# Kernel tuning notes

Hardware: AMD Instinct MI355X
Metric: run time of the kernel (lower is better)

The kernel has to match this reference:

```python
import jax, jax.numpy as jnp
import numpy as np
import math

DIM = 1024
NUM_HEADS = 16
HEAD_DIM = 64
NUM_FEATURES = 128
B, N = 2, 1024


def _sample_orf(rng, num_features, head_dim):
    # Orthogonal Random Features: stack QR-orthogonalized blocks scaled by chi(D) row norms
    blocks = []
    while len(blocks) * head_dim < num_features:
        G = rng.standard_normal((head_dim, head_dim)).astype(np.float32)
        Q, _ = np.linalg.qr(G)
        norms = np.linalg.norm(rng.standard_normal((head_dim, head_dim)).astype(np.float32), axis=1)
        blocks.append(np.diag(norms) @ Q.T)
    return np.concatenate(blocks, axis=0)[:num_features]


def setup_inputs() -> dict:
    key = jax.random.key(0)
    ks = jax.random.split(key, 6)
    s = 1.0 / math.sqrt(DIM)
    x = jax.random.normal(ks[0], (B, N, DIM), dtype=jnp.float32)
    omega = jnp.asarray(_sample_orf(np.random.default_rng(0), NUM_FEATURES, HEAD_DIM))
    Wq = jax.random.normal(ks[1], (DIM, DIM), dtype=jnp.float32) * s
    Wk = jax.random.normal(ks[2], (DIM, DIM), dtype=jnp.float32) * s
    Wv = jax.random.normal(ks[3], (DIM, DIM), dtype=jnp.float32) * s
    Wo = jax.random.normal(ks[4], (DIM, DIM), dtype=jnp.float32) * s
    bo = jax.random.normal(ks[5], (DIM,), dtype=jnp.float32) * 0.01
    return {"x": x, "omega": omega, "Wq": Wq, "Wk": Wk, "Wv": Wv, "Wo": Wo, "bo": bo}


def _phi(x, omega, is_query):
    # x: [B,H,N,D], omega: [M,D] -> [B,H,N,M]
    proj = jnp.einsum('bhnd,md->bhnm', x, omega)
    norm = 0.5 * jnp.sum(x * x, axis=-1, keepdims=True)
    log_phi = proj - norm
    if is_query:
        log_phi = log_phi - jnp.max(log_phi, axis=-1, keepdims=True)
    else:
        log_phi = log_phi - jnp.max(log_phi)
    return jnp.exp(log_phi) / math.sqrt(NUM_FEATURES) + 1e-4


def reference(x, omega, Wq, Wk, Wv, Wo, bo):
    Bx, Nx, _ = x.shape
    H, D = NUM_HEADS, HEAD_DIM

    def split_heads(y):  # [B,N,H*D] -> [B,H,N,D]
        return y.reshape(Bx, Nx, H, D).transpose(0, 2, 1, 3)

    q = split_heads(x @ Wq.T)
    k = split_heads(x @ Wk.T)
    v = split_heads(x @ Wv.T)

    scale = D ** (-0.25)
    phi_q = _phi(q * scale, omega, is_query=True)   # [B,H,N,M]
    phi_k = _phi(k * scale, omega, is_query=False)  # [B,H,N,M]

    # causal linear attention via explicit kv outer-product cumsum (as in source)
    kv = jnp.einsum('bhnm,bhnd->bhnmd', phi_k, v)
    kv_cumsum = jnp.cumsum(kv, axis=2)              # [B,H,N,M,D]
    k_cumsum = jnp.cumsum(phi_k, axis=2)            # [B,H,N,M]
    out = jnp.einsum('bhnm,bhnmd->bhnd', phi_q, kv_cumsum)
    z = 1.0 / (jnp.einsum('bhnm,bhnm->bhn', phi_q, k_cumsum) + 1e-6)
    out = out * z[..., None]

    out = out.transpose(0, 2, 1, 3).reshape(Bx, Nx, H * D)
    return out @ Wo.T + bo
```

## Files before the change

kernel.cpp:

```cpp
#include <hip/hip_runtime.h>
#include <hip/hip_bf16.h>
#include <math.h>

#define DIMS 1024
#define NHEADS 16
#define HDIM 64
#define NFEAT 128
#define BB 2
#define NN 1024
#define BN (BB*NN)
#define NCH 16
#define CSZ 64
#define WW (DIMS*DIMS)
#define QKVN (3*DIMS)

#define SCALE 0.3535533905932738f
#define INV_SQRT_M 0.08838834764831845f

typedef __attribute__((ext_vector_type(8))) _Float16 h8v;
typedef __attribute__((ext_vector_type(8))) short s8v;
typedef __attribute__((ext_vector_type(4))) float f4v;

__device__ __forceinline__ ushort f2h(float x) {
    _Float16 h = (_Float16)x;
    return *(ushort*)&h;
}
__device__ __forceinline__ float h2f(ushort u) {
    _Float16 h = *(_Float16*)&u;
    return (float)h;
}
__device__ __forceinline__ void gload16(const void* g, void* l) {
    __builtin_amdgcn_global_load_lds(
        (const __attribute__((address_space(1))) unsigned int*)g,
        (__attribute__((address_space(3))) unsigned int*)l,
        16, 0, 0);
}

#define NX (BN*DIMS/8)
#define NW (WW/8)
#define NOM (NFEAT*HDIM/8)
__global__ __launch_bounds__(256) void cast_all(const float* __restrict__ x,
                                                const float* __restrict__ Wq,
                                                const float* __restrict__ Wk,
                                                const float* __restrict__ Wv,
                                                const float* __restrict__ Wo,
                                                const float* __restrict__ omega,
                                                ushort* __restrict__ xh,
                                                ushort* __restrict__ wqkvh,
                                                ushort* __restrict__ woh,
                                                ushort* __restrict__ omh) {
    const int i = blockIdx.x * 256 + threadIdx.x;
    const float* src; ushort* dst; int off;
    if (i < NX)               { src = x;     dst = xh;                     off = i; }
    else if (i < NX + NW)     { src = Wq;    dst = wqkvh;                  off = i - NX; }
    else if (i < NX + 2 * NW) { src = Wk;    dst = wqkvh + WW;             off = i - NX - NW; }
    else if (i < NX + 3 * NW) { src = Wv;    dst = wqkvh + 2 * (size_t)WW; off = i - NX - 2 * NW; }
    else if (i < NX + 4 * NW) { src = Wo;    dst = woh;                    off = i - NX - 3 * NW; }
    else                      { src = omega; dst = omh;                    off = i - NX - 4 * NW; }
    float4 a = ((const float4*)src)[2 * (size_t)off];
    float4 b = ((const float4*)src)[2 * (size_t)off + 1];
    float v[8] = {a.x, a.y, a.z, a.w, b.x, b.y, b.z, b.w};
    ushort h8[8];
    #pragma unroll
    for (int j = 0; j < 8; ++j) h8[j] = f2h(v[j]);
    *(s8v*)&dst[(size_t)off * 8] = *(s8v*)&h8[0];
}

template<int BM, bool HOUT>
__global__ __launch_bounds__(256) void gemm_nt_lds(const ushort* __restrict__ A,
                                                   const ushort* __restrict__ B,
                                                   float* __restrict__ C,
                                                   ushort* __restrict__ C16,
                                                   const float* __restrict__ bias,
                                                   int M, int N, int K, int nbx) {
    constexpr int MF = BM / 32;
    constexpr int AI = BM / 64;
    __shared__ __attribute__((aligned(16))) ushort lA[BM][32];
    __shared__ __attribute__((aligned(16))) ushort lB[128][32];
    const int tid = threadIdx.x;
    const int w = tid >> 6, l = tid & 63, lr = l & 15, lg = l >> 4;
    const int wm = (w >> 1) * (BM / 2), wn = (w & 1) * 64;
    const int nwg = gridDim.x;
    const int q8 = nwg >> 3;
    const int neu = (blockIdx.x & 7) * q8 + (blockIdx.x >> 3);
    const int bx = neu % nbx, by = neu / nbx;
    const int bi = bx * BM, bj = by * 128;
    const int srow = l >> 2, scol = (l & 3) * 8;

    f4v acc[MF][4] = {};
    for (int k0 = 0; k0 < K; k0 += 32) {
        #pragma unroll
        for (int i = 0; i < AI; ++i) {
            const int r0 = w * (16 * AI) + i * 16;
            gload16(&A[(size_t)(bi + r0 + srow) * K + k0 + scol], &lA[r0][0]);
        }
        #pragma unroll
        for (int i = 0; i < 2; ++i) {
            const int r0 = w * 32 + i * 16;
            gload16(&B[(size_t)(bj + r0 + srow) * K + k0 + scol], &lB[r0][0]);
        }
        __syncthreads();
        h8v b_[4];
        #pragma unroll
        for (int j = 0; j < 4; ++j) b_[j] = *(h8v*)&lB[wn + j * 16 + lr][lg * 8];
        #pragma unroll
        for (int i = 0; i < MF; ++i) {
            h8v a_ = *(h8v*)&lA[wm + i * 16 + lr][lg * 8];
            #pragma unroll
            for (int j = 0; j < 4; ++j)
                acc[i][j] = __builtin_amdgcn_mfma_f32_16x16x32_f16(a_, b_[j], acc[i][j], 0, 0, 0);
        }
        __syncthreads();
    }
    #pragma unroll
    for (int i = 0; i < MF; ++i)
        #pragma unroll
        for (int j = 0; j < 4; ++j)
            #pragma unroll
            for (int rg = 0; rg < 4; ++rg) {
                const int row = bi + wm + i * 16 + lg * 4 + rg;
                const int col = bj + wn + j * 16 + lr;
                if (HOUT) {
                    C16[(size_t)row * N + col] = f2h(acc[i][j][rg]);
                } else {
                    float r = acc[i][j][rg] + bias[col];
                    C[(size_t)row * N + col] = r;
                }
            }
}

__global__ __launch_bounds__(256) void phi_mfma(const ushort* __restrict__ qkvh,
                                                const ushort* __restrict__ omh,
                                                ushort* __restrict__ phiq,
                                                ushort* __restrict__ plocal,
                                                float* __restrict__ blockmax,
                                                ushort* __restrict__ vt,
                                                ushort* __restrict__ ssum16,
                                                float* __restrict__ kcsum,
                                                float* __restrict__ vsum) {
    __shared__ __attribute__((aligned(16))) ushort lq[64][72];
    __shared__ __attribute__((aligned(16))) ushort lom[128 * 72];
    __shared__ __attribute__((aligned(16))) ushort lktT[128][72];
    __shared__ __attribute__((aligned(16))) ushort lv[64][72];
    __shared__ __attribute__((aligned(16))) ushort lvt[64][72];
    __shared__ float lnorm[64];
    __shared__ float wred[4];
    const int tid = threadIdx.x;
    const int z = blockIdx.z, h = blockIdx.y;
    const int bn0 = blockIdx.x * 64;
    const int w = tid >> 6, l = tid & 63, lr = l & 15, lg = l >> 4;
    const int b = blockIdx.x >> 4, c = blockIdx.x & 15;
    const int bh = b * NHEADS + h;

    {
        const int r = tid >> 2, c0 = (tid & 3) * 16;
        const size_t g = (size_t)(bn0 + r) * QKVN + (size_t)z * DIMS + h * HDIM + c0;
        s8v v0 = *(const s8v*)&qkvh[g];
        s8v v1 = *(const s8v*)&qkvh[g + 8];
        *(s8v*)&lq[r][c0] = v0;
        *(s8v*)&lq[r][c0 + 8] = v1;
        float p = 0.f;
        #pragma unroll
        for (int j = 0; j < 8; ++j) {
            float a = h2f(((ushort*)&v0)[j]); p += a * a;
            float bb2 = h2f(((ushort*)&v1)[j]); p += bb2 * bb2;
        }
        p += __shfl_xor(p, 1); p += __shfl_xor(p, 2);
        if ((tid & 3) == 0) lnorm[r] = p;
    }
    {
        const int m = tid >> 1, c0 = (tid & 1) * 32;
        #pragma unroll
        for (int i = 0; i < 4; ++i)
            *(s8v*)&lom[m * 72 + c0 + i * 8] = *(const s8v*)&omh[m * HDIM + c0 + i * 8];
    }
    if (z == 1) {
        const int r = tid >> 2, c0 = (tid & 3) * 16;
        const size_t g = (size_t)(bn0 + r) * QKVN + 2 * DIMS + h * HDIM + c0;
        *(s8v*)&lv[r][c0]     = *(const s8v*)&qkvh[g];
        *(s8v*)&lv[r][c0 + 8] = *(const s8v*)&qkvh[g + 8];
    }
    __syncthreads();

    f4v acc[8] = {};
    #pragma unroll
    for (int k0 = 0; k0 < 64; k0 += 32) {
        h8v a = *(h8v*)&lq[w * 16 + lr][k0 + lg * 8];
        #pragma unroll
        for (int ct = 0; ct < 8; ++ct) {
            h8v bo = *(h8v*)&lom[(ct * 16 + lr) * 72 + k0 + lg * 8];
            acc[ct] = __builtin_amdgcn_mfma_f32_16x16x32_f16(a, bo, acc[ct], 0, 0, 0);
        }
    }

    const float hs2 = 0.5f * SCALE * SCALE;
    float lvv[4][8];
    #pragma unroll
    for (int rg = 0; rg < 4; ++rg) {
        const int row = w * 16 + lg * 4 + rg;
        const float nh = hs2 * lnorm[row];
        #pragma unroll
        for (int ct = 0; ct < 8; ++ct) lvv[rg][ct] = SCALE * acc[ct][rg] - nh;
    }
    if (z == 1) {
        float bmax = -3.4e38f;
        #pragma unroll
        for (int rg = 0; rg < 4; ++rg)
            #pragma unroll
            for (int ct = 0; ct < 8; ++ct) bmax = fmaxf(bmax, lvv[rg][ct]);
        #pragma unroll
        for (int o = 32; o >= 1; o >>= 1) bmax = fmaxf(bmax, __shfl_xor(bmax, o));
        if (l == 0) wred[w] = bmax;
    }
    __syncthreads();

    if (z == 0) {
        #pragma unroll
        for (int rg = 0; rg < 4; ++rg) {
            const int row = w * 16 + lg * 4 + rg;
            float mx = -3.4e38f;
            #pragma unroll
            for (int ct = 0; ct < 8; ++ct) mx = fmaxf(mx, lvv[rg][ct]);
            #pragma unroll
            for (int o = 8; o >= 1; o >>= 1) mx = fmaxf(mx, __shfl_xor(mx, o));
            #pragma unroll
            for (int ct = 0; ct < 8; ++ct)
                lom[row * 136 + ct * 16 + lr] = f2h(expf(lvv[rg][ct] - mx) * INV_SQRT_M + 1e-4f);
        }
    } else {
        const float bm = fmaxf(fmaxf(wred[0], wred[1]), fmaxf(wred[2], wred[3]));
        if (tid == 0) blockmax[h * 32 + blockIdx.x] = bm;
        #pragma unroll
        for (int rg = 0; rg < 4; ++rg) {
            const int row = w * 16 + lg * 4 + rg;
            #pragma unroll
            for (int ct = 0; ct < 8; ++ct)
                lom[row * 136 + ct * 16 + lr] = f2h(expf(lvv[rg][ct] - bm));
        }
    }
    __syncthreads();

    {
        ushort* dst = (z == 0) ? phiq : plocal;
        const int r = tid >> 2, c0 = (tid & 3) * 32;
        const size_t orow = ((size_t)bh * NN + (blockIdx.x & 15) * 64 + ((bn0 >> 10) ? 0 : 0)
                             + ((size_t)0)) * 0;
        const int br = bn0 + r;
        const int bb2 = br >> 10, n = br & (NN - 1);
        const size_t og = ((size_t)(bb2 * NHEADS + h) * NN + n) * NFEAT;
        #pragma unroll
        for (int i = 0; i < 4; ++i)
            *(s8v*)&dst[og + c0 + i * 8] = *(s8v*)&lom[r * 136 + c0 + i * 8];
        (void)orow;
    }
    if (z == 0) return;

    {
        const int m = tid >> 1, nh2 = (tid & 1) * 32;
        ushort tp[32];
        #pragma unroll
        for (int i = 0; i < 32; ++i) tp[i] = lom[(nh2 + i) * 136 + m];
        #pragma unroll
        for (int i = 0; i < 4; ++i) *(s8v*)&lktT[m][nh2 + i * 8] = *(s8v*)&tp[i * 8];
    }
    {
        const int d = tid >> 2, s0 = (tid & 3) * 16;
        ushort tp[16];
        #pragma unroll
        for (int i = 0; i < 16; ++i) tp[i] = lv[s0 + i][d];
        const size_t tb = ((size_t)bh * HDIM + d) * NN + c * CSZ + (b ? 0 : 0) + s0;
        *(s8v*)&vt[((size_t)bh * HDIM + d) * NN + c * CSZ + s0] = *(s8v*)&tp[0];
        *(s8v*)&vt[((size_t)bh * HDIM + d) * NN + c * CSZ + s0 + 8] = *(s8v*)&tp[8];
        *(s8v*)&lvt[d][s0] = *(s8v*)&tp[0];
        *(s8v*)&lvt[d][s0 + 8] = *(s8v*)&tp[8];
        (void)tb;
    }
    __syncthreads();

    f4v ac2[8] = {};
    #pragma unroll
    for (int k0 = 0; k0 < 64; k0 += 32) {
        h8v a = *(h8v*)&lvt[w * 16 + lr][k0 + lg * 8];
        #pragma unroll
        for (int ct = 0; ct < 8; ++ct) {
            h8v bf = *(h8v*)&lktT[ct * 16 + lr][k0 + lg * 8];
            ac2[ct] = __builtin_amdgcn_mfma_f32_16x16x32_f16(a, bf, ac2[ct], 0, 0, 0);
        }
    }
    const size_t obase = ((size_t)bh * NCH + c) * (HDIM * NFEAT);
    #pragma unroll
    for (int ct = 0; ct < 8; ++ct)
        #pragma unroll
        for (int rg = 0; rg < 4; ++rg) {
            const int d = w * 16 + lg * 4 + rg, m = ct * 16 + lr;
            ssum16[obase + (size_t)d * NFEAT + m] = f2h(ac2[ct][rg]);
        }
    if (tid < 128) {
        float s = 0.f;
        #pragma unroll 8
        for (int i = 0; i < 64; ++i) s += h2f(lktT[tid][i]);
        kcsum[((size_t)bh * NCH + c) * NFEAT + tid] = s;
    }
    if (tid < 64) {
        float s = 0.f;
        #pragma unroll 8
        for (int i = 0; i < 64; ++i) s += h2f(lvt[tid][i]);
        vsum[((size_t)bh * NCH + c) * HDIM + tid] = s;
    }
}

__global__ __launch_bounds__(256) void chunk_prefix(const ushort* __restrict__ ssum16,
                                                    ushort* __restrict__ spre,
                                                    const float* __restrict__ kcsum,
                                                    float* __restrict__ kcpre,
                                                    const float* __restrict__ blockmax,
                                                    const float* __restrict__ vsum) {
    const int bh = blockIdx.y, sl = blockIdx.x;
    const int tid = threadIdx.x;
    const int b = bh >> 4, h = bh & 15;
    __shared__ float gred[4];
    float mx = fmaxf(blockmax[tid], blockmax[tid + 256]);
    #pragma unroll
    for (int o = 32; o >= 1; o >>= 1) mx = fmaxf(mx, __shfl_xor(mx, o));
    if ((tid & 63) == 0) gred[tid >> 6] = mx;
    __syncthreads();
    const float gm = fmaxf(fmaxf(gred[0], gred[1]), fmaxf(gred[2], gred[3]));

    if (sl == 0 && tid < NFEAT) {
        float a = 0.f;
        for (int c = 0; c < NCH; ++c) {
            kcpre[((size_t)bh * NCH + c) * NFEAT + tid] = a;
            const float fac = expf(blockmax[h * 32 + b * 16 + c] - gm) * INV_SQRT_M;
            a += fac * kcsum[((size_t)bh * NCH + c) * NFEAT + tid] + 64.0f * 1e-4f;
        }
    }
    const int base_e = (sl * 256 + tid) * 8;
    const int d = base_e >> 7;
    float acc[8] = {};
    const size_t bb = (size_t)bh * NCH * (HDIM * NFEAT);
    for (int c = 0; c < NCH; ++c) {
        const size_t cb = bb + (size_t)c * (HDIM * NFEAT);
        const float fac = expf(blockmax[h * 32 + b * 16 + c] - gm) * INV_SQRT_M;
        const float vs = vsum[((size_t)bh * NCH + c) * HDIM + d];
        s8v v = *(const s8v*)&ssum16[cb + base_e];
        ushort o[8];
        #pragma unroll
        for (int j = 0; j < 8; ++j) o[j] = f2h(acc[j]);
        *(s8v*)&spre[cb + base_e] = *(s8v*)&o[0];
        #pragma unroll
        for (int j = 0; j < 8; ++j) acc[j] += fac * h2f(((ushort*)&v)[j]) + 1e-4f * vs;
    }
}

__global__ __launch_bounds__(256) void scan_final(const ushort* __restrict__ phiq,
                                                  const ushort* __restrict__ plocal,
                                                  const ushort* __restrict__ vt,
                                                  const ushort* __restrict__ spre,
                                                  const float* __restrict__ kcpre,
                                                  const float* __restrict__ blockmax,
                                                  ushort* __restrict__ att_h) {
    const int c = blockIdx.x, bh = blockIdx.y;
    const int b = bh >> 4, h = bh & 15;
    const int n0 = c * CSZ;
    __shared__ __attribute__((aligned(16))) ushort lq[64][136];
    __shared__ __attribute__((aligned(16))) ushort lk[64][136];
    __shared__ __attribute__((aligned(16))) ushort lvt[64][72];
    __shared__ __attribute__((aligned(16))) ushort lsp[64][136];
    __shared__ __attribute__((aligned(16))) ushort lA[64][72];
    __shared__ float kc[NFEAT];
    __shared__ float zin[64];
    __shared__ float zp[4][64];
    __shared__ float gred[4];
    const int tid = threadIdx.x;

    float mxv = fmaxf(blockmax[tid], blockmax[tid + 256]);
    #pragma unroll
    for (int o = 32; o >= 1; o >>= 1) mxv = fmaxf(mxv, __shfl_xor(mxv, o));
    if ((tid & 63) == 0) gred[tid >> 6] = mxv;
    __syncthreads();
    const float gm = fmaxf(fmaxf(gred[0], gred[1]), fmaxf(gred[2], gred[3]));
    const float fac = expf(blockmax[h * 32 + b * 16 + c] - gm) * INV_SQRT_M;

    const size_t qb = ((size_t)bh * NN + n0) * NFEAT;
    #pragma unroll
    for (int i = 0; i < 4; ++i) {
        const int idx = tid + 256 * i;
        const int r = idx >> 4, cs = (idx & 15) * 8;
        *(s8v*)&lq[r][cs] = *(const s8v*)&phiq[qb + (size_t)r * NFEAT + cs];
        s8v pv = *(const s8v*)&plocal[qb + (size_t)r * NFEAT + cs];
        ushort t[8];
        #pragma unroll
        for (int j = 0; j < 8; ++j) t[j] = f2h(h2f(((ushort*)&pv)[j]) * fac + 1e-4f);
        *(s8v*)&lk[r][cs] = *(s8v*)&t[0];
    }
    const size_t sb = ((size_t)bh * NCH + c) * (HDIM * NFEAT);
    #pragma unroll
    for (int i = 0; i < 4; ++i) {
        const int idx = tid + 256 * i;
        const int r = idx >> 4, cs = (idx & 15) * 8;
        *(s8v*)&lsp[r][cs] = *(const s8v*)&spre[sb + (size_t)r * NFEAT + cs];
    }
    {
        const int d = tid >> 2, s = (tid & 3) * 16;
        const size_t g = ((size_t)bh * HDIM + d) * NN + n0 + s;
        *(s8v*)&lvt[d][s]     = *(const s8v*)&vt[g];
        *(s8v*)&lvt[d][s + 8] = *(const s8v*)&vt[g + 8];
    }
    if (tid < NFEAT) kc[tid] = kcpre[((size_t)bh * NCH + c) * NFEAT + tid];
    __syncthreads();

    const int w = tid >> 6, l = tid & 63, lr = l & 15, lg = l >> 4;

    f4v a4[4] = {};
    #pragma unroll
    for (int k0 = 0; k0 < 128; k0 += 32) {
        h8v av = *(h8v*)&lq[w * 16 + lr][k0 + lg * 8];
        #pragma unroll
        for (int ct = 0; ct < 4; ++ct) {
            h8v bv = *(h8v*)&lk[ct * 16 + lr][k0 + lg * 8];
            a4[ct] = __builtin_amdgcn_mfma_f32_16x16x32_f16(av, bv, a4[ct], 0, 0, 0);
        }
    }
    float zi[4] = {0.f, 0.f, 0.f, 0.f};
    #pragma unroll
    for (int ct = 0; ct < 4; ++ct) {
        #pragma unroll
        for (int rg = 0; rg < 4; ++rg) {
            const int row = w * 16 + lg * 4 + rg;
            const int col = ct * 16 + lr;
            const float val = (col <= row) ? a4[ct][rg] : 0.f;
            const ushort hq = f2h(val);
            zi[rg] += h2f(hq);
            lA[row][col] = hq;
        }
    }
    #pragma unroll
    for (int rg = 0; rg < 4; ++rg) {
        float z = zi[rg];
        z += __shfl_xor(z, 1); z += __shfl_xor(z, 2);
        z += __shfl_xor(z, 4); z += __shfl_xor(z, 8);
        if (lr == 0) zin[w * 16 + lg * 4 + rg] = z;
    }
    {
        const int row = tid & 63, qq = tid >> 6;
        float s = 0.f;
        #pragma unroll 8
        for (int m = 0; m < 32; ++m) s += h2f(lq[row][qq * 32 + m]) * kc[qq * 32 + m];
        zp[qq][row] = s;
    }
    __syncthreads();

    f4v o4[4] = {};
    #pragma unroll
    for (int k0 = 0; k0 < 64; k0 += 32) {
        h8v av = *(h8v*)&lA[w * 16 + lr][k0 + lg * 8];
        #pragma unroll
        for (int ct = 0; ct < 4; ++ct) {
            h8v bv = *(h8v*)&lvt[ct * 16 + lr][k0 + lg * 8];
            o4[ct] = __builtin_amdgcn_mfma_f32_16x16x32_f16(av, bv, o4[ct], 0, 0, 0);
        }
    }
    #pragma unroll
    for (int k0 = 0; k0 < 128; k0 += 32) {
        h8v av = *(h8v*)&lq[w * 16 + lr][k0 + lg * 8];
        #pragma unroll
        for (int ct = 0; ct < 4; ++ct) {
            h8v bv = *(h8v*)&lsp[ct * 16 + lr][k0 + lg * 8];
            o4[ct] = __builtin_amdgcn_mfma_f32_16x16x32_f16(av, bv, o4[ct], 0, 0, 0);
        }
    }
    #pragma unroll
    for (int rg = 0; rg < 4; ++rg) {
        const int row = w * 16 + lg * 4 + rg;
        const float z = zin[row] + zp[0][row] + zp[1][row] + zp[2][row] + zp[3][row] + 1e-6f;
        const float rz = 1.f / z;
        #pragma unroll
        for (int ct = 0; ct < 4; ++ct) {
            const int d = ct * 16 + lr;
            att_h[((size_t)(b * NN + n0 + row)) * DIMS + h * HDIM + d] = f2h(o4[ct][rg] * rz);
        }
    }
}

extern "C" void kernel_launch(void* const* d_in, const int* in_sizes, int n_in,
                              void* d_out, int out_size, void* d_ws, size_t ws_size,
                              hipStream_t stream) {
    const float* x     = (const float*)d_in[0];
    const float* omega = (const float*)d_in[1];
    const float* Wq    = (const float*)d_in[2];
    const float* Wk    = (const float*)d_in[3];
    const float* Wv    = (const float*)d_in[4];
    const float* Wo    = (const float*)d_in[5];
    const float* bo    = (const float*)d_in[6];
    float* out = (float*)d_out;

    const size_t PROJ = (size_t)BN * DIMS;
    const size_t PHI  = (size_t)BB * NHEADS * NN * NFEAT;
    ushort* qkvh    = (ushort*)d_ws;
    ushort* xh      = qkvh + (size_t)BN * QKVN;
    ushort* wqkvh   = xh + PROJ;
    ushort* woh     = wqkvh + (size_t)QKVN * DIMS;
    ushort* omh     = woh + WW;
    ushort* phiq_h  = omh + NFEAT * HDIM;
    ushort* plocal  = phiq_h + PHI;
    ushort* vt_h    = plocal + PHI;
    ushort* ssum16  = vt_h + PROJ;
    ushort* spre_h  = ssum16 + PHI;
    ushort* att_hb  = spre_h + PHI;
    float*  kcsum   = (float*)(att_hb + PROJ);
    float*  kcpre   = kcsum + 32 * NCH * NFEAT;
    float*  blockmax= kcpre + 32 * NCH * NFEAT;
    float*  vsum    = blockmax + 512;

    cast_all<<<(NX + 4 * NW + NOM) / 256, 256, 0, stream>>>(x, Wq, Wk, Wv, Wo, omega,
                                                            xh, wqkvh, woh, omh);

    gemm_nt_lds<64, true><<<(BN / 64) * (QKVN / 128), 256, 0, stream>>>(
        xh, wqkvh, nullptr, qkvh, nullptr, BN, QKVN, DIMS, BN / 64);

    dim3 pg(BN / 64, NHEADS, 2);
    phi_mfma<<<pg, 256, 0, stream>>>(qkvh, omh, phiq_h, plocal, blockmax,
                                     vt_h, ssum16, kcsum, vsum);

    chunk_prefix<<<dim3(4, BB * NHEADS), 256, 0, stream>>>(ssum16, spre_h, kcsum, kcpre,
                                                           blockmax, vsum);
    dim3 cg(NCH, BB * NHEADS);
    scan_final<<<cg, 256, 0, stream>>>(phiq_h, plocal, vt_h, spre_h, kcpre,
                                       blockmax, att_hb);

    gemm_nt_lds<64, false><<<(BN / 64) * (DIMS / 128), 256, 0, stream>>>(
        att_hb, woh, out, nullptr, bo, BN, DIMS, DIMS, BN / 64);
}
```

Baseline: 89.02 us.

## Fuse chunk prefix into scan_final and widen GEMM K-tile with swizzled LDS

Removes the separate chunk_prefix kernel: each scan_final block now recomputes its own exclusive prefix of the chunk state sums and key sums directly from ssum16/kcsum, saving a launch and the spre/kcpre round trip through memory. The price is redundant work, since later chunks re-read and accumulate up to 15 prior chunk states, which adds quadratic reads and per-thread register pressure (32 float accumulators). Separately, the GEMM K-tile is doubled from 32 to 64 with an XOR-swizzled LDS layout to halve barriers per K and cut bank conflicts. Some dead address code is also cleaned up.

```diff
diff --git a/kernel.cpp b/kernel.cpp
--- a/kernel.cpp
+++ b/kernel.cpp
@@ -74,9 +74,9 @@
                                                    const float* __restrict__ bias,
                                                    int M, int N, int K, int nbx) {
     constexpr int MF = BM / 32;
-    constexpr int AI = BM / 64;
-    __shared__ __attribute__((aligned(16))) ushort lA[BM][32];
-    __shared__ __attribute__((aligned(16))) ushort lB[128][32];
+    constexpr int AI = BM / 32;
+    __shared__ __attribute__((aligned(16))) ushort lA[BM][64];
+    __shared__ __attribute__((aligned(16))) ushort lB[128][64];
     const int tid = threadIdx.x;
     const int w = tid >> 6, l = tid & 63, lr = l & 15, lg = l >> 4;
     const int wm = (w >> 1) * (BM / 2), wn = (w & 1) * 64;
@@ -85,30 +85,35 @@
     const int neu = (blockIdx.x & 7) * q8 + (blockIdx.x >> 3);
     const int bx = neu % nbx, by = neu / nbx;
     const int bi = bx * BM, bj = by * 128;
-    const int srow = l >> 2, scol = (l & 3) * 8;
+    const int srow = l >> 3;
+    const int scol = ((l & 7) ^ (l >> 3)) * 8;
 
     f4v acc[MF][4] = {};
-    for (int k0 = 0; k0 < K; k0 += 32) {
+    for (int k0 = 0; k0 < K; k0 += 64) {
         #pragma unroll
         for (int i = 0; i < AI; ++i) {
-            const int r0 = w * (16 * AI) + i * 16;
+            const int r0 = w * (8 * AI) + i * 8;
             gload16(&A[(size_t)(bi + r0 + srow) * K + k0 + scol], &lA[r0][0]);
         }
         #pragma unroll
-        for (int i = 0; i < 2; ++i) {
-            const int r0 = w * 32 + i * 16;
+        for (int i = 0; i < 4; ++i) {
+            const int r0 = w * 32 + i * 8;
             gload16(&B[(size_t)(bj + r0 + srow) * K + k0 + scol], &lB[r0][0]);
         }
         __syncthreads();
-        h8v b_[4];
-        #pragma unroll
-        for (int j = 0; j < 4; ++j) b_[j] = *(h8v*)&lB[wn + j * 16 + lr][lg * 8];
-        #pragma unroll
-        for (int i = 0; i < MF; ++i) {
-            h8v a_ = *(h8v*)&lA[wm + i * 16 + lr][lg * 8];
-            #pragma unroll
-            for (int j = 0; j < 4; ++j)
-                acc[i][j] = __builtin_amdgcn_mfma_f32_16x16x32_f16(a_, b_[j], acc[i][j], 0, 0, 0);
+        #pragma unroll
+        for (int kk = 0; kk < 2; ++kk) {
+            const int soff = ((kk * 4 + lg) ^ (lr & 7)) * 8;
+            h8v b_[4];
+            #pragma unroll
+            for (int j = 0; j < 4; ++j) b_[j] = *(h8v*)&lB[wn + j * 16 + lr][soff];
+            #pragma unroll
+            for (int i = 0; i < MF; ++i) {
+                h8v a_ = *(h8v*)&lA[wm + i * 16 + lr][soff];
+                #pragma unroll
+                for (int j = 0; j < 4; ++j)
+                    acc[i][j] = __builtin_amdgcn_mfma_f32_16x16x32_f16(a_, b_[j], acc[i][j], 0, 0, 0);
+            }
         }
         __syncthreads();
     }
@@ -243,15 +248,12 @@
     {
         ushort* dst = (z == 0) ? phiq : plocal;
         const int r = tid >> 2, c0 = (tid & 3) * 32;
-        const size_t orow = ((size_t)bh * NN + (blockIdx.x & 15) * 64 + ((bn0 >> 10) ? 0 : 0)
-                             + ((size_t)0)) * 0;
         const int br = bn0 + r;
         const int bb2 = br >> 10, n = br & (NN - 1);
         const size_t og = ((size_t)(bb2 * NHEADS + h) * NN + n) * NFEAT;
         #pragma unroll
         for (int i = 0; i < 4; ++i)
             *(s8v*)&dst[og + c0 + i * 8] = *(s8v*)&lom[r * 136 + c0 + i * 8];
-        (void)orow;
     }
     if (z == 0) return;
 
@@ -268,12 +270,11 @@
         ushort tp[16];
         #pragma unroll
         for (int i = 0; i < 16; ++i) tp[i] = lv[s0 + i][d];
-        const size_t tb = ((size_t)bh * HDIM + d) * NN + c * CSZ + (b ? 0 : 0) + s0;
-        *(s8v*)&vt[((size_t)bh * HDIM + d) * NN + c * CSZ + s0] = *(s8v*)&tp[0];
-        *(s8v*)&vt[((size_t)bh * HDIM + d) * NN + c * CSZ + s0 + 8] = *(s8v*)&tp[8];
+        const size_t tb = ((size_t)bh * HDIM + d) * NN + c * CSZ + s0;
+        *(s8v*)&vt[tb] = *(s8v*)&tp[0];
+        *(s8v*)&vt[tb + 8] = *(s8v*)&tp[8];
         *(s8v*)&lvt[d][s0] = *(s8v*)&tp[0];
         *(s8v*)&lvt[d][s0 + 8] = *(s8v*)&tp[8];
-        (void)tb;
     }
     __syncthreads();
 
@@ -309,54 +310,12 @@
     }
 }
 
-__global__ __launch_bounds__(256) void chunk_prefix(const ushort* __restrict__ ssum16,
-                                                    ushort* __restrict__ spre,
-                                                    const float* __restrict__ kcsum,
-                                                    float* __restrict__ kcpre,
-                                                    const float* __restrict__ blockmax,
-                                                    const float* __restrict__ vsum) {
-    const int bh = blockIdx.y, sl = blockIdx.x;
-    const int tid = threadIdx.x;
-    const int b = bh >> 4, h = bh & 15;
-    __shared__ float gred[4];
-    float mx = fmaxf(blockmax[tid], blockmax[tid + 256]);
-    #pragma unroll
-    for (int o = 32; o >= 1; o >>= 1) mx = fmaxf(mx, __shfl_xor(mx, o));
-    if ((tid & 63) == 0) gred[tid >> 6] = mx;
-    __syncthreads();
-    const float gm = fmaxf(fmaxf(gred[0], gred[1]), fmaxf(gred[2], gred[3]));
-
-    if (sl == 0 && tid < NFEAT) {
-        float a = 0.f;
-        for (int c = 0; c < NCH; ++c) {
-            kcpre[((size_t)bh * NCH + c) * NFEAT + tid] = a;
-            const float fac = expf(blockmax[h * 32 + b * 16 + c] - gm) * INV_SQRT_M;
-            a += fac * kcsum[((size_t)bh * NCH + c) * NFEAT + tid] + 64.0f * 1e-4f;
-        }
-    }
-    const int base_e = (sl * 256 + tid) * 8;
-    const int d = base_e >> 7;
-    float acc[8] = {};
-    const size_t bb = (size_t)bh * NCH * (HDIM * NFEAT);
-    for (int c = 0; c < NCH; ++c) {
-        const size_t cb = bb + (size_t)c * (HDIM * NFEAT);
-        const float fac = expf(blockmax[h * 32 + b * 16 + c] - gm) * INV_SQRT_M;
-        const float vs = vsum[((size_t)bh * NCH + c) * HDIM + d];
-        s8v v = *(const s8v*)&ssum16[cb + base_e];
-        ushort o[8];
-        #pragma unroll
-        for (int j = 0; j < 8; ++j) o[j] = f2h(acc[j]);
-        *(s8v*)&spre[cb + base_e] = *(s8v*)&o[0];
-        #pragma unroll
-        for (int j = 0; j < 8; ++j) acc[j] += fac * h2f(((ushort*)&v)[j]) + 1e-4f * vs;
-    }
-}
-
 __global__ __launch_bounds__(256) void scan_final(const ushort* __restrict__ phiq,
                                                   const ushort* __restrict__ plocal,
                                                   const ushort* __restrict__ vt,
-                                                  const ushort* __restrict__ spre,
-                                                  const float* __restrict__ kcpre,
+                                                  const ushort* __restrict__ ssum16,
+                                                  const float* __restrict__ kcsum,
+                                                  const float* __restrict__ vsum,
                                                   const float* __restrict__ blockmax,
                                                   ushort* __restrict__ att_h) {
     const int c = blockIdx.x, bh = blockIdx.y;
@@ -393,12 +352,36 @@
         for (int j = 0; j < 8; ++j) t[j] = f2h(h2f(((ushort*)&pv)[j]) * fac + 1e-4f);
         *(s8v*)&lk[r][cs] = *(s8v*)&t[0];
     }
-    const size_t sb = ((size_t)bh * NCH + c) * (HDIM * NFEAT);
-    #pragma unroll
-    for (int i = 0; i < 4; ++i) {
-        const int idx = tid + 256 * i;
-        const int r = idx >> 4, cs = (idx & 15) * 8;
-        *(s8v*)&lsp[r][cs] = *(const s8v*)&spre[sb + (size_t)r * NFEAT + cs];
+    {
+        const int d = tid >> 2;
+        const int m0 = (tid & 3) * 32;
+        float acc[32] = {};
+        float vs_tot = 0.f;
+        for (int cp = 0; cp < c; ++cp) {
+            const float facp = expf(blockmax[h * 32 + b * 16 + cp] - gm) * INV_SQRT_M;
+            vs_tot += vsum[((size_t)bh * NCH + cp) * HDIM + d];
+            const size_t cb = ((size_t)bh * NCH + cp) * (HDIM * NFEAT) + (size_t)d * NFEAT + m0;
+            #pragma unroll
+            for (int i = 0; i < 4; ++i) {
+                s8v v = *(const s8v*)&ssum16[cb + i * 8];
+                #pragma unroll
+                for (int j = 0; j < 8; ++j) acc[i * 8 + j] += facp * h2f(((ushort*)&v)[j]);
+            }
+        }
+        const float vadd = 1e-4f * vs_tot;
+        ushort o[32];
+        #pragma unroll
+        for (int i = 0; i < 32; ++i) o[i] = f2h(acc[i] + vadd);
+        #pragma unroll
+        for (int i = 0; i < 4; ++i) *(s8v*)&lsp[d][m0 + i * 8] = *(s8v*)&o[i * 8];
+    }
+    if (tid < NFEAT) {
+        float a = 0.f;
+        for (int cp = 0; cp < c; ++cp) {
+            const float facp = expf(blockmax[h * 32 + b * 16 + cp] - gm) * INV_SQRT_M;
+            a += facp * kcsum[((size_t)bh * NCH + cp) * NFEAT + tid] + 64.0f * 1e-4f;
+        }
+        kc[tid] = a;
     }
     {
         const int d = tid >> 2, s = (tid & 3) * 16;
@@ -406,7 +389,6 @@
         *(s8v*)&lvt[d][s]     = *(const s8v*)&vt[g];
         *(s8v*)&lvt[d][s + 8] = *(const s8v*)&vt[g + 8];
     }
-    if (tid < NFEAT) kc[tid] = kcpre[((size_t)bh * NCH + c) * NFEAT + tid];
     __syncthreads();
 
     const int w = tid >> 6, l = tid & 63, lr = l & 15, lg = l >> 4;
@@ -505,11 +487,9 @@
     ushort* plocal  = phiq_h + PHI;
     ushort* vt_h    = plocal + PHI;
     ushort* ssum16  = vt_h + PROJ;
-    ushort* spre_h  = ssum16 + PHI;
-    ushort* att_hb  = spre_h + PHI;
+    ushort* att_hb  = ssum16 + PHI;
     float*  kcsum   = (float*)(att_hb + PROJ);
-    float*  kcpre   = kcsum + 32 * NCH * NFEAT;
-    float*  blockmax= kcpre + 32 * NCH * NFEAT;
+    float*  blockmax= kcsum + 32 * NCH * NFEAT;
     float*  vsum    = blockmax + 512;
 
     cast_all<<<(NX + 4 * NW + NOM) / 256, 256, 0, stream>>>(x, Wq, Wk, Wv, Wo, omega,
@@ -522,10 +502,8 @@
     phi_mfma<<<pg, 256, 0, stream>>>(qkvh, omh, phiq_h, plocal, blockmax,
                                      vt_h, ssum16, kcsum, vsum);
 
-    chunk_prefix<<<dim3(4, BB * NHEADS), 256, 0, stream>>>(ssum16, spre_h, kcsum, kcpre,
-                                                           blockmax, vsum);
     dim3 cg(NCH, BB * NHEADS);
-    scan_final<<<cg, 256, 0, stream>>>(phiq_h, plocal, vt_h, spre_h, kcpre,
+    scan_final<<<cg, 256, 0, stream>>>(phiq_h, plocal, vt_h, ssum16, kcsum, vsum,
                                        blockmax, att_hb);
 
     gemm_nt_lds<64, false><<<(BN / 64) * (DIMS / 128), 256, 0, stream>>>(
```

Result: faster. 86.26 us (-3.1%).
